# Kernel optimization log

Hardware: AMD Instinct MI355X
Metric: run time of the kernel (lower is better)

The kernel has to match this reference:

```python
import jax, jax.numpy as jnp
import numpy as np

B, T, F, K = 32, 1500, 512, 31
QBITS = 8
EPS = 1e-5


def fake_quant(x, bits=QBITS):
    """Symmetric per-tensor fake quantization (scale from dynamic max-abs),
    with straight-through estimator so gradients pass through unchanged."""
    qmax = 2.0 ** (bits - 1) - 1.0  # 127 for 8 bits
    scale = jnp.maximum(jnp.max(jnp.abs(x)) / qmax, 1e-8)
    q = jnp.clip(jnp.round(x / scale), -qmax - 1.0, qmax) * scale
    return x + jax.lax.stop_gradient(q - x)


def setup_inputs() -> dict:
    key = jax.random.key(0)
    ks = jax.random.split(key, 5)
    x = jax.random.normal(ks[0], (B, T, F), dtype=jnp.float32)
    W1 = jax.random.normal(ks[1], (2 * F, F), dtype=jnp.float32) * (1.0 / np.sqrt(F))
    b1 = jnp.zeros((2 * F,), jnp.float32)
    dw_w = jax.random.normal(ks[2], (F, 1, K), dtype=jnp.float32) * (1.0 / np.sqrt(K))
    dw_b = jnp.zeros((F,), jnp.float32)
    W2 = jax.random.normal(ks[3], (F, F), dtype=jnp.float32) * (1.0 / np.sqrt(F))
    b2 = jnp.zeros((F,), jnp.float32)
    return {
        "x": x,
        "ln_gamma": jnp.ones((F,), jnp.float32),
        "ln_beta": jnp.zeros((F,), jnp.float32),
        "W1": W1, "b1": b1,
        "dw_w": dw_w, "dw_b": dw_b,
        "bn_gamma": jnp.ones((F,), jnp.float32),
        "bn_beta": jnp.zeros((F,), jnp.float32),
        "W2": W2, "b2": b2,
    }


def _forward(x, ln_gamma, ln_beta, W1, b1, dw_w, dw_b, bn_gamma, bn_beta, W2, b2):
    # LayerNorm over last dim F
    mu = jnp.mean(x, axis=-1, keepdims=True)
    var = jnp.mean(jnp.square(x - mu), axis=-1, keepdims=True)
    t = (x - mu) * jax.lax.rsqrt(var + EPS) * ln_gamma + ln_beta

    # pconv1 in-quant -> quantized pointwise conv1 (Linear F -> 2F) -> out-quant
    t = fake_quant(t)
    t = jnp.einsum("btf,gf->btg", t, fake_quant(W1)) + b1
    t = fake_quant(t)

    # GLU over last dim: [B,T,2F] -> [B,T,F]
    a, g = jnp.split(t, 2, axis=-1)
    t = a * jax.nn.sigmoid(g)

    # depthwise conv on [B,F,T]
    t = jnp.transpose(t, (0, 2, 1))  # [B,F,T]
    t = fake_quant(t)
    t = jax.lax.conv_general_dilated(
        t, fake_quant(dw_w),
        window_strides=(1,),
        padding=[((K - 1) // 2, (K - 1) // 2)],
        feature_group_count=F,
        dimension_numbers=("NCH", "OIH", "NCH"),
    ) + dw_b[None, :, None]
    t = fake_quant(t)

    # BatchNorm1d over channel dim (stats over batch and time), training-style batch stats
    bmu = jnp.mean(t, axis=(0, 2), keepdims=True)
    bvar = jnp.mean(jnp.square(t - bmu), axis=(0, 2), keepdims=True)
    t = (t - bmu) * jax.lax.rsqrt(bvar + EPS) * bn_gamma[None, :, None] + bn_beta[None, :, None]

    t = jnp.transpose(t, (0, 2, 1))  # [B,T,F]
    t = jax.nn.silu(t)

    # pconv2 in-quant -> quantized pointwise conv2 (Linear F -> F) -> out-quant
    t = fake_quant(t)
    t = jnp.einsum("btf,gf->btg", t, fake_quant(W2)) + b2
    t = fake_quant(t)
    return t  # dropout is identity (p=0 / eval)


def reference(x, ln_gamma, ln_beta, W1, b1, dw_w, dw_b, bn_gamma, bn_beta, W2, b2):
    return _forward(x, ln_gamma, ln_beta, W1, b1, dw_w, dw_b, bn_gamma, bn_beta, W2, b2)
```

## Files before the change

kernel.cpp:

```cpp
#include <hip/hip_runtime.h>
#include <stdint.h>

typedef __bf16 bf16;
typedef __bf16   bf16x4 __attribute__((ext_vector_type(4)));
typedef __bf16   bf16x8 __attribute__((ext_vector_type(8)));
typedef short    s16x8  __attribute__((ext_vector_type(8)));
typedef float    fx4    __attribute__((ext_vector_type(4)));

#define NB 32
#define NT 1500
#define NF 512
#define NM (NB*NT)
#define KW 31
#define EPSF 1e-5f

__device__ __forceinline__ float dscale(const float* a) {
  return fmaxf(a[0] * (1.0f/127.0f), 1e-8f);
}
__device__ __forceinline__ float fq_int(float x, float inv_s) {
  return fminf(fmaxf(rintf(x*inv_s), -128.0f), 127.0f);
}
__device__ __forceinline__ void block_amax(float v, float* dst) {
  __shared__ float red[8];
  #pragma unroll
  for (int o = 32; o > 0; o >>= 1) v = fmaxf(v, __shfl_xor(v, o));
  if ((threadIdx.x & 63) == 0) red[threadIdx.x >> 6] = v;
  __syncthreads();
  if (threadIdx.x == 0) {
    int nw = blockDim.x >> 6;
    float m = red[0];
    for (int i = 1; i < nw; i++) m = fmaxf(m, red[i]);
    atomicMax((unsigned int*)dst, __float_as_uint(m));
  }
}

__device__ __forceinline__ float amax_loop(const float* p, long n4, int bid, int gsz) {
  float am = 0.f;
  long i = (long)bid * blockDim.x + threadIdx.x;
  long stride = (long)gsz * blockDim.x;
  for (; i < n4; i += stride) {
    fx4 v = ((const fx4*)p)[i];
    #pragma unroll
    for (int j = 0; j < 4; j++) am = fmaxf(am, fabsf(v[j]));
  }
  return am;
}
__global__ void absmax_w(const float* __restrict__ W1, const float* __restrict__ W2,
                         const float* __restrict__ dwp, float* a) {
  int bx = blockIdx.x;
  float am; float* dst;
  if (bx < 256)      { am = amax_loop(W1,  131072, bx,       256); dst = a + 1; }
  else if (bx < 384) { am = amax_loop(W2,  65536,  bx - 256, 128); dst = a + 2; }
  else               { am = amax_loop(dwp, 3968,   bx - 384, 8);   dst = a + 3; }
  block_amax(am, dst);
}

__global__ void quant_pack(const float* __restrict__ src, bf16* __restrict__ dst,
                           int R, const float* amax) {
  float inv_s = 1.0f / dscale(amax);
  int total = R * 64;
  for (int t = blockIdx.x*blockDim.x + threadIdx.x; t < total; t += gridDim.x*blockDim.x) {
    int r = t >> 6, q8 = t & 63;
    const float* s = src + (size_t)r*512 + q8*8;
    fx4 v0 = *(const fx4*)s, v1 = *(const fx4*)(s+4);
    bf16x8 o;
    #pragma unroll
    for (int j = 0; j < 4; j++) { o[j] = (bf16)fq_int(v0[j], inv_s); o[4+j] = (bf16)fq_int(v1[j], inv_s); }
    int r16 = r >> 4, m16 = r & 15, kb = q8 >> 2, quad = q8 & 3;
    size_t chunk = ((size_t)r16*16 + kb)*64 + quad*16 + m16;
    ((bf16x8*)dst)[chunk] = o;
  }
}

__global__ void quant_deq_f32(float* __restrict__ p, long n4, const float* amax) {
  float s = dscale(amax);
  float inv_s = 1.0f / s;
  long i = (long)blockIdx.x * blockDim.x + threadIdx.x;
  long stride = (long)gridDim.x * blockDim.x;
  for (; i < n4; i += stride) {
    fx4 v = ((fx4*)p)[i];
    fx4 o;
    #pragma unroll
    for (int j = 0; j < 4; j++) o[j] = fq_int(v[j], inv_s) * s;
    ((fx4*)p)[i] = o;
  }
}

__global__ void ln_amax_k(const float* __restrict__ x, const float* __restrict__ g,
                          const float* __restrict__ be, float* amax) {
  int lane = threadIdx.x & 63;
  int wavesTotal = (gridDim.x * blockDim.x) >> 6;
  int wave = ((blockIdx.x * blockDim.x) + threadIdx.x) >> 6;
  fx4 g0 = ((const fx4*)g)[2*lane],  g1 = ((const fx4*)g)[2*lane+1];
  fx4 b0 = ((const fx4*)be)[2*lane], b1v = ((const fx4*)be)[2*lane+1];
  float gf[8], bff[8];
  #pragma unroll
  for (int j = 0; j < 4; j++) { gf[j] = g0[j]; gf[4+j] = g1[j]; bff[j] = b0[j]; bff[4+j] = b1v[j]; }
  float am = 0.f;
  for (int row = wave; row < NM; row += wavesTotal) {
    const fx4* xr = (const fx4*)(x + (long)row*NF);
    fx4 x0 = xr[2*lane], x1 = xr[2*lane+1];
    float xf[8]; float s = 0.f;
    #pragma unroll
    for (int j = 0; j < 4; j++) { xf[j] = x0[j]; xf[4+j] = x1[j]; }
    #pragma unroll
    for (int j = 0; j < 8; j++) s += xf[j];
    #pragma unroll
    for (int o = 32; o > 0; o >>= 1) s += __shfl_xor(s, o);
    float mu = s * (1.0f/NF);
    float vs = 0.f;
    #pragma unroll
    for (int j = 0; j < 8; j++) { float d = xf[j]-mu; vs += d*d; }
    #pragma unroll
    for (int o = 32; o > 0; o >>= 1) vs += __shfl_xor(vs, o);
    float inv = rsqrtf(vs*(1.0f/NF) + EPSF);
    #pragma unroll
    for (int j = 0; j < 8; j++) {
      float v = (xf[j]-mu)*inv*gf[j] + bff[j];
      am = fmaxf(am, fabsf(v));
    }
  }
  block_amax(am, amax);
}

__global__ void ln_pack_k(const float* __restrict__ x, const float* __restrict__ g,
                          const float* __restrict__ be, bf16* __restrict__ dst,
                          const float* amax) {
  int lane = threadIdx.x & 63;
  int wavesTotal = (gridDim.x * blockDim.x) >> 6;
  int wave = ((blockIdx.x * blockDim.x) + threadIdx.x) >> 6;
  float inv_s = 1.0f / dscale(amax);
  fx4 g0 = ((const fx4*)g)[2*lane],  g1 = ((const fx4*)g)[2*lane+1];
  fx4 b0 = ((const fx4*)be)[2*lane], b1v = ((const fx4*)be)[2*lane+1];
  float gf[8], bff[8];
  #pragma unroll
  for (int j = 0; j < 4; j++) { gf[j] = g0[j]; gf[4+j] = g1[j]; bff[j] = b0[j]; bff[4+j] = b1v[j]; }
  for (int row = wave; row < NM; row += wavesTotal) {
    const fx4* xr = (const fx4*)(x + (long)row*NF);
    fx4 x0 = xr[2*lane], x1 = xr[2*lane+1];
    float xf[8]; float s = 0.f;
    #pragma unroll
    for (int j = 0; j < 4; j++) { xf[j] = x0[j]; xf[4+j] = x1[j]; }
    #pragma unroll
    for (int j = 0; j < 8; j++) s += xf[j];
    #pragma unroll
    for (int o = 32; o > 0; o >>= 1) s += __shfl_xor(s, o);
    float mu = s * (1.0f/NF);
    float vs = 0.f;
    #pragma unroll
    for (int j = 0; j < 8; j++) { float d = xf[j]-mu; vs += d*d; }
    #pragma unroll
    for (int o = 32; o > 0; o >>= 1) vs += __shfl_xor(vs, o);
    float inv = rsqrtf(vs*(1.0f/NF) + EPSF);
    bf16x8 o8;
    #pragma unroll
    for (int j = 0; j < 8; j++) {
      float v = (xf[j]-mu)*inv*gf[j] + bff[j];
      o8[j] = (bf16)fq_int(v, inv_s);
    }
    int r16 = row >> 4, m16 = row & 15;
    size_t chunk = ((size_t)r16*16 + (lane>>2))*64 + (lane&3)*16 + m16;
    ((bf16x8*)dst)[chunk] = o8;
  }
}

template<int NBN, int MODE>
__global__ __launch_bounds__(256) void gemm_k(
    const bf16* __restrict__ A, const bf16* __restrict__ Bt,
    const float* __restrict__ bias, float* __restrict__ C,
    const float* amaxA, const float* amaxB, float* amaxC) {
  const int N = NBN * 128;
  int id = blockIdx.x;
  int bn = (id >> 3) % NBN;
  int bm = 8 * (id / (8 * NBN)) + (id & 7);
  if (bm >= 375) return;
  int lane = threadIdx.x & 63;
  int w = threadIdx.x >> 6;
  int wm = w >> 1, wn = w & 1;
  int quad = lane >> 4;
  int m16 = lane & 15;

  __shared__ __align__(16) float ebuf[2][32][132];

  fx4 acc[4][4];
  #pragma unroll
  for (int i = 0; i < 4; i++)
    #pragma unroll
    for (int j = 0; j < 4; j++) acc[i][j] = fx4{0.f,0.f,0.f,0.f};

  const bf16* pA[4];
  const bf16* pB[4];
  #pragma unroll
  for (int i = 0; i < 4; i++)
    pA[i] = A + ((size_t)(bm*8 + wm*4 + i)*16)*512 + lane*8;
  #pragma unroll
  for (int j = 0; j < 4; j++)
    pB[j] = Bt + ((size_t)(bn*8 + wn*4 + j)*16)*512 + lane*8;

  s16x8 aC[4], bC[4], aN[4], bN[4];
  #pragma unroll
  for (int i = 0; i < 4; i++) aC[i] = *(const s16x8*)(pA[i]);
  #pragma unroll
  for (int j = 0; j < 4; j++) bC[j] = *(const s16x8*)(pB[j]);

  #pragma unroll
  for (int kb = 0; kb < 16; kb++) {
    if (kb < 15) {
      #pragma unroll
      for (int i = 0; i < 4; i++) aN[i] = *(const s16x8*)(pA[i] + (kb+1)*512);
      #pragma unroll
      for (int j = 0; j < 4; j++) bN[j] = *(const s16x8*)(pB[j] + (kb+1)*512);
    }
    #pragma unroll
    for (int i = 0; i < 4; i++)
      #pragma unroll
      for (int j = 0; j < 4; j++) {
        if (MODE == 0)
          acc[i][j] = __builtin_amdgcn_mfma_f32_16x16x32_bf16(aC[i], bC[j], acc[i][j], 0, 0, 0);
        else
          acc[i][j] = __builtin_amdgcn_mfma_f32_16x16x32_bf16(bC[j], aC[i], acc[i][j], 0, 0, 0);
      }
    __builtin_amdgcn_sched_group_barrier(0x20, 8, 0);
    __builtin_amdgcn_sched_group_barrier(0x8, 16, 0);
    if (kb < 15) {
      #pragma unroll
      for (int i = 0; i < 4; i++) { aC[i] = aN[i]; bC[i] = bN[i]; }
    }
  }

  float ab = dscale(amaxA) * dscale(amaxB);
  float am = 0.f;
  const int h     = (MODE == 0) ? wn : wm;
  const int other = (MODE == 0) ? wm : wn;

  #pragma unroll
  for (int rnd = 0; rnd < 2; rnd++) {
    __syncthreads();
    if (MODE == 0) {
      #pragma unroll
      for (int jj = 0; jj < 2; jj++) {
        int j = rnd*2 + jj;
        int col = bn*128 + wn*64 + j*16 + m16;
        float bv = bias[col];
        #pragma unroll
        for (int i = 0; i < 4; i++) {
          fx4 o;
          #pragma unroll
          for (int rr = 0; rr < 4; rr++) {
            float v = acc[i][j][rr]*ab + bv;
            am = fmaxf(am, fabsf(v)); o[rr] = v;
          }
          *(fx4*)&ebuf[h][jj*16 + m16][wm*64 + i*16 + quad*4] = o;
        }
      }
    } else {
      #pragma unroll
      for (int ii = 0; ii < 2; ii++) {
        int i = rnd*2 + ii;
        #pragma unroll
        for (int j = 0; j < 4; j++) {
          int n0 = bn*128 + wn*64 + j*16 + quad*4;
          fx4 bv = *(const fx4*)(bias + n0);
          fx4 o;
          #pragma unroll
          for (int rr = 0; rr < 4; rr++) {
            float v = acc[i][j][rr]*ab + bv[rr];
            am = fmaxf(am, fabsf(v)); o[rr] = v;
          }
          *(fx4*)&ebuf[h][ii*16 + m16][wn*64 + j*16 + quad*4] = o;
        }
      }
    }
    __syncthreads();
    #pragma unroll
    for (int it = 0; it < 8; it++) {
      int lrow = other*16 + it*2 + (lane >> 5);
      int cf = (lane & 31) * 4;
      fx4 o = *(const fx4*)&ebuf[h][lrow][cf];
      int orow = ((MODE == 0) ? bn*128 : bm*128) + h*64 + rnd*32 + lrow;
      size_t base = (MODE == 0) ? ((size_t)orow*NM + (size_t)bm*128 + cf)
                                : ((size_t)orow*N  + (size_t)bn*128 + cf);
      *(fx4*)(C + base) = o;
    }
  }
  block_amax(am, amaxC);
}

__global__ void glu_k(const float* __restrict__ uT, float* __restrict__ v,
                      const float* amaxU, float* amaxV) {
  float s = dscale(amaxU);
  float inv_s = 1.0f / s;
  float am = 0.f;
  const int tid = threadIdx.x;
  const int npairs = (NB*NF)/2;
  for (int pr = blockIdx.x; pr < npairs; pr += gridDim.x) {
    int row0 = pr*2;
    for (int i = tid; i < 750; i += 256) {
      int r2 = (i >= 375) ? 1 : 0;
      int c = i - 375*r2;
      int row = row0 + r2;
      int b = row >> 9, f = row & (NF-1);
      long bt = (long)b*NT + c*4;
      fx4 a = *(const fx4*)(uT + (long)f*NM + bt);
      fx4 g = *(const fx4*)(uT + (long)(f+NF)*NM + bt);
      fx4 o;
      #pragma unroll
      for (int j = 0; j < 4; j++) {
        float av = fq_int(a[j], inv_s) * s;
        float gv = fq_int(g[j], inv_s) * s;
        float val = av * (1.0f/(1.0f + expf(-gv)));
        am = fmaxf(am, fabsf(val));
        o[j] = val;
      }
      *(fx4*)(v + (long)row*NT + c*4) = o;
    }
  }
  block_amax(am, amaxV);
}

__global__ void dwconv_k(const float* __restrict__ v, const float* __restrict__ w,
                         const float* __restrict__ wb, float* __restrict__ y,
                         const float* amaxV, const float* amaxW, float* amaxY) {
  __shared__ float z[2][1568];
  __shared__ float wl[2][32];
  float sv = dscale(amaxV); float inv_sv = 1.0f/sv;
  float sw = dscale(amaxW); float inv_sw = 1.0f/sw;
  float am = 0.f;
  const int tid = threadIdx.x;
  const int rr = tid >> 7;
  const int cl = tid & 127;
  const int npairs = (NB*NF)/2;
  for (int pr = blockIdx.x; pr < npairs; pr += gridDim.x) {
    int row0 = pr*2;
    __syncthreads();
    if (tid < 64) {
      int r2 = tid >> 5, k = tid & 31;
      if (k < KW) {
        int f = (row0 + r2) & (NF-1);
        wl[r2][k] = fq_int(w[f*KW + k], inv_sw) * sw;
      }
    }
    if (tid < 128) {
      int r2 = tid >> 6, jj = tid & 63;
      if (jj < 16) z[r2][jj] = 0.f;
      else         z[r2][1500 + jj] = 0.f;
    }
    const fx4* vp = (const fx4*)(v + (long)row0 * NT);
    for (int i = tid; i < 750; i += 256) {
      fx4 q = vp[i];
      int r2 = (i >= 375) ? 1 : 0;
      int ii = i - 375*r2;
      fx4 o;
      #pragma unroll
      for (int j = 0; j < 4; j++) o[j] = fq_int(q[j], inv_sv) * sv;
      *(fx4*)&z[r2][16 + 4*ii] = o;
    }
    __syncthreads();
    float wr[KW];
    #pragma unroll
    for (int k = 0; k < KW; k++) wr[k] = wl[rr][k];
    float bias = wb[(row0 + rr) & (NF-1)];
    long base = (long)(row0 + rr) * NT;
    #pragma unroll
    for (int pass = 0; pass < 3; pass++) {
      int c = cl + pass*128;
      if (c < 375) {
        int t0 = c*4;
        fx4 win[9];
        #pragma unroll
        for (int i = 0; i < 9; i++) win[i] = *(const fx4*)&z[rr][t0 + 4*i];
        float acc0 = bias, acc1 = bias, acc2 = bias, acc3 = bias;
        #pragma unroll
        for (int k = 0; k < KW; k++) {
          float wk = wr[k];
          acc0 += win[(k+1)>>2][(k+1)&3] * wk;
          acc1 += win[(k+2)>>2][(k+2)&3] * wk;
          acc2 += win[(k+3)>>2][(k+3)&3] * wk;
          acc3 += win[(k+4)>>2][(k+4)&3] * wk;
        }
        fx4 o = {acc0, acc1, acc2, acc3};
        #pragma unroll
        for (int j = 0; j < 4; j++) am = fmaxf(am, fabsf(o[j]));
        *(fx4*)&y[base + t0] = o;
      }
    }
  }
  block_amax(am, amaxY);
}

__global__ void bnstats_part_k(const float* __restrict__ y, const float* amaxY,
                               int* s1a, int* s2a, unsigned* qmxa, unsigned* qmna) {
  float sy = dscale(amaxY); float inv_sy = 1.0f/sy;
  int f = blockIdx.x & 511;
  int part = blockIdx.x >> 9;
  int s1 = 0, s2 = 0, qmn = 127, qmx = -128;
  for (int b = part*8; b < part*8 + 8; b++) {
    const fx4* base = (const fx4*)(y + ((long)b*NF + f)*NT);
    for (int i = threadIdx.x; i < NT/4; i += blockDim.x) {
      fx4 v = base[i];
      #pragma unroll
      for (int j = 0; j < 4; j++) {
        int q = (int)fq_int(v[j], inv_sy);
        s1 += q; s2 += q*q;
        qmn = min(qmn, q); qmx = max(qmx, q);
      }
    }
  }
  #pragma unroll
  for (int o = 32; o > 0; o >>= 1) {
    s1 += __shfl_xor(s1, o); s2 += __shfl_xor(s2, o);
    qmn = min(qmn, __shfl_xor(qmn, o)); qmx = max(qmx, __shfl_xor(qmx, o));
  }
  __shared__ int rs1[4], rs2[4], rmn[4], rmx[4];
  if ((threadIdx.x & 63) == 0) {
    int wv = threadIdx.x >> 6;
    rs1[wv] = s1; rs2[wv] = s2; rmn[wv] = qmn; rmx[wv] = qmx;
  }
  __syncthreads();
  if (threadIdx.x == 0) {
    int S1 = rs1[0]+rs1[1]+rs1[2]+rs1[3];
    int S2 = rs2[0]+rs2[1]+rs2[2]+rs2[3];
    int mn = min(min(rmn[0],rmn[1]), min(rmn[2],rmn[3]));
    int mx = max(max(rmx[0],rmx[1]), max(rmx[2],rmx[3]));
    atomicAdd(s1a + f, S1);
    atomicAdd(s2a + f, S2);
    atomicMax(qmxa + f, (unsigned)(mx + 128));
    atomicMax(qmna + f, (unsigned)(127 - mn));
  }
}

__global__ void bnfin_k(const int* __restrict__ s1a, const int* __restrict__ s2a,
                        const unsigned* __restrict__ qmxa, const unsigned* __restrict__ qmna,
                        const float* amaxY, const float* __restrict__ bg,
                        const float* __restrict__ bb,
                        float* bn_mean, float* bn_rinv, float* amaxP) {
  int f = blockIdx.x;
  float sy = dscale(amaxY);
  __shared__ float sh_mean, sh_rinv; __shared__ int sh_qmn, sh_qmx;
  if (threadIdx.x == 0) {
    long long S1 = s1a[f];
    long long S2 = s2a[f];
    double s = (double)sy;
    double mean = (double)S1 * s / (double)NM;
    double var  = (double)S2 * s * s / (double)NM - mean*mean;
    float fm = (float)mean;
    float fr = rsqrtf((float)var + EPSF);
    bn_mean[f] = fm; bn_rinv[f] = fr;
    sh_mean = fm; sh_rinv = fr;
    sh_qmx = (int)qmxa[f] - 128;
    sh_qmn = 127 - (int)qmna[f];
  }
  __syncthreads();
  float pm = 0.f;
  int q = sh_qmn + (int)threadIdx.x;
  if (q <= sh_qmx) {
    float zq = (float)q * sy;
    float val = (zq - sh_mean)*sh_rinv*bg[f] + bb[f];
    val = val / (1.0f + expf(-val));
    pm = fabsf(val);
  }
  block_amax(pm, amaxP);
}

__global__ void bnsilu_pack_k(const float* __restrict__ y, const float* __restrict__ bg,
                              const float* __restrict__ bb, const float* amaxY,
                              const float* bn_mean, const float* bn_rinv,
                              bf16* __restrict__ pq, const float* amaxP) {
  __shared__ float lds[32][33];
  float sy = dscale(amaxY); float inv_sy = 1.0f/sy;
  float inv_sp = 1.0f / dscale(amaxP);
  int tx = threadIdx.x & 31, ty = threadIdx.x >> 5;
  const int TTILES = (NT + 31)/32;
  const int ntile = NB * (NF/32) * TTILES;
  for (int tile = blockIdx.x; tile < ntile; tile += gridDim.x) {
    int b = tile / ((NF/32)*TTILES);
    int rem = tile % ((NF/32)*TTILES);
    int fT = rem / TTILES, tT = rem % TTILES;
    int f0 = fT*32, t0 = tT*32;
    __syncthreads();
    #pragma unroll
    for (int sI = 0; sI < 4; sI++) {
      int f = f0 + ty + sI*8;
      int t = t0 + tx;
      if (t < NT) {
        float zq = fq_int(y[((long)b*NF + f)*NT + t], inv_sy) * sy;
        float val = (zq - bn_mean[f])*bn_rinv[f]*bg[f] + bb[f];
        val = val / (1.0f + expf(-val));
        lds[tx][ty + sI*8] = val;
      }
    }
    __syncthreads();
    if (threadIdx.x < 128) {
      int r = threadIdx.x >> 2;
      int c = threadIdx.x & 3;
      int t = t0 + r;
      if (t < NT) {
        bf16x8 o8;
        #pragma unroll
        for (int j = 0; j < 8; j++) o8[j] = (bf16)fq_int(lds[r][c*8 + j], inv_sp);
        long bt = (long)b*NT + t;
        int q8 = (f0 >> 3) + c;
        size_t chunk = ((size_t)(bt>>4)*16 + (q8>>2))*64 + (q8&3)*16 + (bt&15);
        ((bf16x8*)pq)[chunk] = o8;
      }
    }
  }
}

extern "C" void kernel_launch(void* const* d_in, const int* in_sizes, int n_in,
                              void* d_out, int out_size, void* d_ws, size_t ws_size,
                              hipStream_t stream) {
  const float* x  = (const float*)d_in[0];
  const float* lg = (const float*)d_in[1];
  const float* lb = (const float*)d_in[2];
  const float* W1 = (const float*)d_in[3];
  const float* b1 = (const float*)d_in[4];
  const float* dw = (const float*)d_in[5];
  const float* db = (const float*)d_in[6];
  const float* bg = (const float*)d_in[7];
  const float* bb = (const float*)d_in[8];
  const float* W2 = (const float*)d_in[9];
  const float* b2 = (const float*)d_in[10];
  float* out = (float*)d_out;

  char* ws = (char*)d_ws;
  float* amax    = (float*)ws;
  float* bn_mean = (float*)(ws + 1024);
  float* bn_rinv = (float*)(ws + 4096);
  int*      s1a  = (int*)(ws + 8192);
  int*      s2a  = (int*)(ws + 10240);
  unsigned* qmxa = (unsigned*)(ws + 12288);
  unsigned* qmna = (unsigned*)(ws + 14336);
  char* H = ws + 16384;
  float* uT    = (float*)H;
  bf16*  t_q   = (bf16*)(H + 196608000);
  float* y     = (float*)H;
  bf16*  p_q   = (bf16*)(H + 196608000);
  bf16*  W1q   = (bf16*)(H + 245760000);
  bf16*  W2q   = (bf16*)(H + 246808576);
  float* v = (float*)d_out;
  float* r = (float*)d_out;

  hipMemsetAsync(ws, 0, 16384, stream);

  absmax_w<<<392, 256, 0, stream>>>(W1, W2, dw, amax);
  quant_pack<<<256, 256, 0, stream>>>(W1, W1q, 1024, amax+1);
  quant_pack<<<128, 256, 0, stream>>>(W2, W2q, 512,  amax+2);

  ln_amax_k<<<1536, 256, 0, stream>>>(x, lg, lb, amax+0);
  ln_pack_k<<<3072, 256, 0, stream>>>(x, lg, lb, t_q, amax+0);
  gemm_k<8,0><<<3008, 256, 0, stream>>>(t_q, W1q, b1, uT, amax+0, amax+1, amax+4);
  glu_k<<<4096, 256, 0, stream>>>(uT, v, amax+4, amax+5);
  dwconv_k<<<2048, 256, 0, stream>>>(v, dw, db, y, amax+5, amax+3, amax+6);
  bnstats_part_k<<<2048, 256, 0, stream>>>(y, amax+6, s1a, s2a, qmxa, qmna);
  bnfin_k<<<512, 256, 0, stream>>>(s1a, s2a, qmxa, qmna, amax+6, bg, bb, bn_mean, bn_rinv, amax+7);
  bnsilu_pack_k<<<4096, 256, 0, stream>>>(y, bg, bb, amax+6, bn_mean, bn_rinv, p_q, amax+7);
  gemm_k<4,1><<<1504, 256, 0, stream>>>(p_q, W2q, b2, r, amax+7, amax+2, amax+8);
  quant_deq_f32<<<2048, 256, 0, stream>>>(out, 24576000/4, amax+8);
}
```

Baseline: 600.9 us.

## Stage GEMM operands through LDS with triple-buffered direct global-to-LDS loads

The GEMM main loop no longer loads A/B fragments straight from global memory into registers. It now issues asynchronous global_load_lds copies into a 3-deep shared-memory ring and synchronises with explicit vmcnt waits and barriers. The goal is to keep more loads in flight, lower register pressure and hide memory latency, at the cost of two block barriers per k-step. Separately, the dwconv launch grid grows from 2048 to 8192 blocks, which only works if that kernel already loops in a grid-stride style.

```diff
diff --git a/kernel.cpp b/kernel.cpp
--- a/kernel.cpp
+++ b/kernel.cpp
@@ -180,7 +180,7 @@
   int quad = lane >> 4;
   int m16 = lane & 15;
 
-  __shared__ __align__(16) float ebuf[2][32][132];
+  __shared__ __align__(16) char smem[49152];
 
   fx4 acc[4][4];
   #pragma unroll
@@ -188,45 +188,58 @@
     #pragma unroll
     for (int j = 0; j < 4; j++) acc[i][j] = fx4{0.f,0.f,0.f,0.f};
 
-  const bf16* pA[4];
-  const bf16* pB[4];
-  #pragma unroll
-  for (int i = 0; i < 4; i++)
-    pA[i] = A + ((size_t)(bm*8 + wm*4 + i)*16)*512 + lane*8;
-  #pragma unroll
-  for (int j = 0; j < 4; j++)
-    pB[j] = Bt + ((size_t)(bn*8 + wn*4 + j)*16)*512 + lane*8;
-
-  s16x8 aC[4], bC[4], aN[4], bN[4];
-  #pragma unroll
-  for (int i = 0; i < 4; i++) aC[i] = *(const s16x8*)(pA[i]);
-  #pragma unroll
-  for (int j = 0; j < 4; j++) bC[j] = *(const s16x8*)(pB[j]);
+  const bf16* gA = A  + (size_t)(bm*8)*16*512;
+  const bf16* gB = Bt + (size_t)(bn*8)*16*512;
+
+  auto issue = [&](int kb) {
+    int b = kb % 3;
+    #pragma unroll
+    for (int q = 0; q < 4; q++) {
+      int p = w*4 + q;
+      const bf16* src = (p < 8)
+          ? (gA + (size_t)p*8192     + (size_t)kb*512 + lane*8)
+          : (gB + (size_t)(p-8)*8192 + (size_t)kb*512 + lane*8);
+      __builtin_amdgcn_global_load_lds(
+          (const __attribute__((address_space(1))) void*)src,
+          (__attribute__((address_space(3))) void*)(smem + b*16384 + p*1024 + lane*16),
+          16, 0, 0);
+    }
+  };
+
+  issue(0); issue(1); issue(2);
 
   #pragma unroll
   for (int kb = 0; kb < 16; kb++) {
-    if (kb < 15) {
-      #pragma unroll
-      for (int i = 0; i < 4; i++) aN[i] = *(const s16x8*)(pA[i] + (kb+1)*512);
-      #pragma unroll
-      for (int j = 0; j < 4; j++) bN[j] = *(const s16x8*)(pB[j] + (kb+1)*512);
-    }
+    if (kb <= 13)      asm volatile("s_waitcnt vmcnt(8)" ::: "memory");
+    else if (kb == 14) asm volatile("s_waitcnt vmcnt(4)" ::: "memory");
+    else               asm volatile("s_waitcnt vmcnt(0)" ::: "memory");
+    __builtin_amdgcn_sched_barrier(0);
+    __builtin_amdgcn_s_barrier();
+    __builtin_amdgcn_sched_barrier(0);
+    char* buf = smem + (kb % 3)*16384;
+    s16x8 aF[4], bF[4];
+    #pragma unroll
+    for (int i = 0; i < 4; i++) aF[i] = *(const s16x8*)(buf + (wm*4 + i)*1024 + lane*16);
+    #pragma unroll
+    for (int j = 0; j < 4; j++) bF[j] = *(const s16x8*)(buf + (8 + wn*4 + j)*1024 + lane*16);
     #pragma unroll
     for (int i = 0; i < 4; i++)
       #pragma unroll
       for (int j = 0; j < 4; j++) {
         if (MODE == 0)
-          acc[i][j] = __builtin_amdgcn_mfma_f32_16x16x32_bf16(aC[i], bC[j], acc[i][j], 0, 0, 0);
+          acc[i][j] = __builtin_amdgcn_mfma_f32_16x16x32_bf16(aF[i], bF[j], acc[i][j], 0, 0, 0);
         else
-          acc[i][j] = __builtin_amdgcn_mfma_f32_16x16x32_bf16(bC[j], aC[i], acc[i][j], 0, 0, 0);
-      }
-    __builtin_amdgcn_sched_group_barrier(0x20, 8, 0);
-    __builtin_amdgcn_sched_group_barrier(0x8, 16, 0);
-    if (kb < 15) {
-      #pragma unroll
-      for (int i = 0; i < 4; i++) { aC[i] = aN[i]; bC[i] = bN[i]; }
-    }
-  }
+          acc[i][j] = __builtin_amdgcn_mfma_f32_16x16x32_bf16(bF[j], aF[i], acc[i][j], 0, 0, 0);
+      }
+    asm volatile("s_waitcnt lgkmcnt(0)" ::: "memory");
+    __builtin_amdgcn_sched_barrier(0);
+    __builtin_amdgcn_s_barrier();
+    __builtin_amdgcn_sched_barrier(0);
+    if (kb + 3 < 16) issue(kb + 3);
+  }
+  __syncthreads();
+
+  float (*ebuf)[32][132] = (float (*)[32][132])smem;
 
   float ab = dscale(amaxA) * dscale(amaxB);
   float am = 0.f;
@@ -551,7 +564,7 @@
   ln_pack_k<<<3072, 256, 0, stream>>>(x, lg, lb, t_q, amax+0);
   gemm_k<8,0><<<3008, 256, 0, stream>>>(t_q, W1q, b1, uT, amax+0, amax+1, amax+4);
   glu_k<<<4096, 256, 0, stream>>>(uT, v, amax+4, amax+5);
-  dwconv_k<<<2048, 256, 0, stream>>>(v, dw, db, y, amax+5, amax+3, amax+6);
+  dwconv_k<<<8192, 256, 0, stream>>>(v, dw, db, y, amax+5, amax+3, amax+6);
   bnstats_part_k<<<2048, 256, 0, stream>>>(y, amax+6, s1a, s2a, qmxa, qmna);
   bnfin_k<<<512, 256, 0, stream>>>(s1a, s2a, qmxa, qmna, amax+6, bg, bb, bn_mean, bn_rinv, amax+7);
   bnsilu_pack_k<<<4096, 256, 0, stream>>>(y, bg, bb, amax+6, bn_mean, bn_rinv, p_q, amax+7);
```

New measurement: 723.6 us. +20.4%, slower.

## Switch quantized GEMMs from bf16 MFMA to int8 MFMA with packed layouts

Applied to the files above, without the earlier changes.

Quantized activations and weights are now packed as int8 instead of bf16 integer values. Both GEMMs use the i32 16x16x64 int8 MFMA and convert the integer accumulators to float in the epilogue. This halves operand bytes and the number of K iterations, and int8 MFMA has higher peak throughput than bf16. The explicit register double-buffering and scheduling barriers are removed, which may expose load latency, and the depthwise conv grid is enlarged.

```diff
diff --git a/kernel.cpp b/kernel.cpp
--- a/kernel.cpp
+++ b/kernel.cpp
@@ -2,10 +2,9 @@
 #include <stdint.h>
 
 typedef __bf16 bf16;
-typedef __bf16   bf16x4 __attribute__((ext_vector_type(4)));
-typedef __bf16   bf16x8 __attribute__((ext_vector_type(8)));
-typedef short    s16x8  __attribute__((ext_vector_type(8)));
 typedef float    fx4    __attribute__((ext_vector_type(4)));
+typedef int      ix2    __attribute__((ext_vector_type(2)));
+typedef int      ix4    __attribute__((ext_vector_type(4)));
 
 #define NB 32
 #define NT 1500
@@ -55,20 +54,25 @@
   block_amax(am, dst);
 }
 
-__global__ void quant_pack(const float* __restrict__ src, bf16* __restrict__ dst,
-                           int R, const float* amax) {
+__global__ void quant_pack_i8(const float* __restrict__ src, char* __restrict__ dst,
+                              int R, const float* amax) {
   float inv_s = 1.0f / dscale(amax);
-  int total = R * 64;
+  int total = R * 32;
   for (int t = blockIdx.x*blockDim.x + threadIdx.x; t < total; t += gridDim.x*blockDim.x) {
-    int r = t >> 6, q8 = t & 63;
-    const float* s = src + (size_t)r*512 + q8*8;
-    fx4 v0 = *(const fx4*)s, v1 = *(const fx4*)(s+4);
-    bf16x8 o;
-    #pragma unroll
-    for (int j = 0; j < 4; j++) { o[j] = (bf16)fq_int(v0[j], inv_s); o[4+j] = (bf16)fq_int(v1[j], inv_s); }
-    int r16 = r >> 4, m16 = r & 15, kb = q8 >> 2, quad = q8 & 3;
-    size_t chunk = ((size_t)r16*16 + kb)*64 + quad*16 + m16;
-    ((bf16x8*)dst)[chunk] = o;
+    int r = t >> 5, q16 = t & 31;
+    const float* s = src + (size_t)r*512 + q16*16;
+    ix4 o;
+    #pragma unroll
+    for (int g = 0; g < 4; g++) {
+      fx4 v = *(const fx4*)(s + g*4);
+      int wrd = 0;
+      #pragma unroll
+      for (int j = 0; j < 4; j++) wrd |= ((int)fq_int(v[j], inv_s) & 0xff) << (8*j);
+      o[g] = wrd;
+    }
+    int r16 = r >> 4, m16 = r & 15, kb = q16 >> 2, quad = q16 & 3;
+    size_t chunk = ((size_t)r16*8 + kb)*64 + quad*16 + m16;
+    ((ix4*)dst)[chunk] = o;
   }
 }
 
@@ -124,7 +128,7 @@
 }
 
 __global__ void ln_pack_k(const float* __restrict__ x, const float* __restrict__ g,
-                          const float* __restrict__ be, bf16* __restrict__ dst,
+                          const float* __restrict__ be, char* __restrict__ dst,
                           const float* amax) {
   int lane = threadIdx.x & 63;
   int wavesTotal = (gridDim.x * blockDim.x) >> 6;
@@ -152,21 +156,25 @@
     #pragma unroll
     for (int o = 32; o > 0; o >>= 1) vs += __shfl_xor(vs, o);
     float inv = rsqrtf(vs*(1.0f/NF) + EPSF);
-    bf16x8 o8;
-    #pragma unroll
-    for (int j = 0; j < 8; j++) {
+    int lo = 0, hi = 0;
+    #pragma unroll
+    for (int j = 0; j < 4; j++) {
       float v = (xf[j]-mu)*inv*gf[j] + bff[j];
-      o8[j] = (bf16)fq_int(v, inv_s);
-    }
-    int r16 = row >> 4, m16 = row & 15;
-    size_t chunk = ((size_t)r16*16 + (lane>>2))*64 + (lane&3)*16 + m16;
-    ((bf16x8*)dst)[chunk] = o8;
+      lo |= ((int)fq_int(v, inv_s) & 0xff) << (8*j);
+    }
+    #pragma unroll
+    for (int j = 0; j < 4; j++) {
+      float v = (xf[4+j]-mu)*inv*gf[4+j] + bff[4+j];
+      hi |= ((int)fq_int(v, inv_s) & 0xff) << (8*j);
+    }
+    size_t chunk = ((size_t)(row>>4)*8 + (lane>>3))*64 + ((lane>>1)&3)*16 + (row&15);
+    *(ix2*)(dst + chunk*16 + (lane&1)*8) = ix2{lo, hi};
   }
 }
 
 template<int NBN, int MODE>
 __global__ __launch_bounds__(256) void gemm_k(
-    const bf16* __restrict__ A, const bf16* __restrict__ Bt,
+    const char* __restrict__ A, const char* __restrict__ Bt,
     const float* __restrict__ bias, float* __restrict__ C,
     const float* amaxA, const float* amaxB, float* amaxC) {
   const int N = NBN * 128;
@@ -182,50 +190,37 @@
 
   __shared__ __align__(16) float ebuf[2][32][132];
 
-  fx4 acc[4][4];
+  ix4 acc[4][4];
   #pragma unroll
   for (int i = 0; i < 4; i++)
     #pragma unroll
-    for (int j = 0; j < 4; j++) acc[i][j] = fx4{0.f,0.f,0.f,0.f};
-
-  const bf16* pA[4];
-  const bf16* pB[4];
+    for (int j = 0; j < 4; j++) acc[i][j] = ix4{0,0,0,0};
+
+  const char* pA[4];
+  const char* pB[4];
   #pragma unroll
   for (int i = 0; i < 4; i++)
-    pA[i] = A + ((size_t)(bm*8 + wm*4 + i)*16)*512 + lane*8;
+    pA[i] = A + (size_t)(bm*8 + wm*4 + i)*8192 + lane*16;
   #pragma unroll
   for (int j = 0; j < 4; j++)
-    pB[j] = Bt + ((size_t)(bn*8 + wn*4 + j)*16)*512 + lane*8;
-
-  s16x8 aC[4], bC[4], aN[4], bN[4];
-  #pragma unroll
-  for (int i = 0; i < 4; i++) aC[i] = *(const s16x8*)(pA[i]);
-  #pragma unroll
-  for (int j = 0; j < 4; j++) bC[j] = *(const s16x8*)(pB[j]);
-
-  #pragma unroll
-  for (int kb = 0; kb < 16; kb++) {
-    if (kb < 15) {
-      #pragma unroll
-      for (int i = 0; i < 4; i++) aN[i] = *(const s16x8*)(pA[i] + (kb+1)*512);
-      #pragma unroll
-      for (int j = 0; j < 4; j++) bN[j] = *(const s16x8*)(pB[j] + (kb+1)*512);
-    }
+    pB[j] = Bt + (size_t)(bn*8 + wn*4 + j)*8192 + lane*16;
+
+  #pragma unroll
+  for (int kb = 0; kb < 8; kb++) {
+    ix4 aF[4], bF[4];
+    #pragma unroll
+    for (int i = 0; i < 4; i++) aF[i] = *(const ix4*)(pA[i] + kb*1024);
+    #pragma unroll
+    for (int j = 0; j < 4; j++) bF[j] = *(const ix4*)(pB[j] + kb*1024);
     #pragma unroll
     for (int i = 0; i < 4; i++)
       #pragma unroll
       for (int j = 0; j < 4; j++) {
         if (MODE == 0)
-          acc[i][j] = __builtin_amdgcn_mfma_f32_16x16x32_bf16(aC[i], bC[j], acc[i][j], 0, 0, 0);
+          acc[i][j] = __builtin_amdgcn_mfma_i32_16x16x64_i8(aF[i], bF[j], acc[i][j], 0, 0, 0);
         else
-          acc[i][j] = __builtin_amdgcn_mfma_f32_16x16x32_bf16(bC[j], aC[i], acc[i][j], 0, 0, 0);
-      }
-    __builtin_amdgcn_sched_group_barrier(0x20, 8, 0);
-    __builtin_amdgcn_sched_group_barrier(0x8, 16, 0);
-    if (kb < 15) {
-      #pragma unroll
-      for (int i = 0; i < 4; i++) { aC[i] = aN[i]; bC[i] = bN[i]; }
-    }
+          acc[i][j] = __builtin_amdgcn_mfma_i32_16x16x64_i8(bF[j], aF[i], acc[i][j], 0, 0, 0);
+      }
   }
 
   float ab = dscale(amaxA) * dscale(amaxB);
@@ -247,7 +242,7 @@
           fx4 o;
           #pragma unroll
           for (int rr = 0; rr < 4; rr++) {
-            float v = acc[i][j][rr]*ab + bv;
+            float v = (float)acc[i][j][rr]*ab + bv;
             am = fmaxf(am, fabsf(v)); o[rr] = v;
           }
           *(fx4*)&ebuf[h][jj*16 + m16][wm*64 + i*16 + quad*4] = o;
@@ -264,7 +259,7 @@
           fx4 o;
           #pragma unroll
           for (int rr = 0; rr < 4; rr++) {
-            float v = acc[i][j][rr]*ab + bv[rr];
+            float v = (float)acc[i][j][rr]*ab + bv[rr];
             am = fmaxf(am, fabsf(v)); o[rr] = v;
           }
           *(fx4*)&ebuf[h][ii*16 + m16][wn*64 + j*16 + quad*4] = o;
@@ -465,7 +460,7 @@
 __global__ void bnsilu_pack_k(const float* __restrict__ y, const float* __restrict__ bg,
                               const float* __restrict__ bb, const float* amaxY,
                               const float* bn_mean, const float* bn_rinv,
-                              bf16* __restrict__ pq, const float* amaxP) {
+                              char* __restrict__ pq, const float* amaxP) {
   __shared__ float lds[32][33];
   float sy = dscale(amaxY); float inv_sy = 1.0f/sy;
   float inv_sp = 1.0f / dscale(amaxP);
@@ -495,13 +490,17 @@
       int c = threadIdx.x & 3;
       int t = t0 + r;
       if (t < NT) {
-        bf16x8 o8;
-        #pragma unroll
-        for (int j = 0; j < 8; j++) o8[j] = (bf16)fq_int(lds[r][c*8 + j], inv_sp);
+        int lo = 0, hi = 0;
+        #pragma unroll
+        for (int j = 0; j < 4; j++)
+          lo |= ((int)fq_int(lds[r][c*8 + j],     inv_sp) & 0xff) << (8*j);
+        #pragma unroll
+        for (int j = 0; j < 4; j++)
+          hi |= ((int)fq_int(lds[r][c*8 + 4 + j], inv_sp) & 0xff) << (8*j);
         long bt = (long)b*NT + t;
         int q8 = (f0 >> 3) + c;
-        size_t chunk = ((size_t)(bt>>4)*16 + (q8>>2))*64 + (q8&3)*16 + (bt&15);
-        ((bf16x8*)pq)[chunk] = o8;
+        size_t chunk = ((size_t)(bt>>4)*8 + (q8>>3))*64 + ((q8>>1)&3)*16 + (bt&15);
+        *(ix2*)(pq + chunk*16 + (q8&1)*8) = ix2{lo, hi};
       }
     }
   }
@@ -533,25 +532,25 @@
   unsigned* qmna = (unsigned*)(ws + 14336);
   char* H = ws + 16384;
   float* uT    = (float*)H;
-  bf16*  t_q   = (bf16*)(H + 196608000);
+  char*  t_q   = H + 196608000;
   float* y     = (float*)H;
-  bf16*  p_q   = (bf16*)(H + 196608000);
-  bf16*  W1q   = (bf16*)(H + 245760000);
-  bf16*  W2q   = (bf16*)(H + 246808576);
+  char*  p_q   = H + 221184000;
+  char*  W1q   = H + 245760000;
+  char*  W2q   = H + 246284288;
   float* v = (float*)d_out;
   float* r = (float*)d_out;
 
   hipMemsetAsync(ws, 0, 16384, stream);
 
   absmax_w<<<392, 256, 0, stream>>>(W1, W2, dw, amax);
-  quant_pack<<<256, 256, 0, stream>>>(W1, W1q, 1024, amax+1);
-  quant_pack<<<128, 256, 0, stream>>>(W2, W2q, 512,  amax+2);
+  quant_pack_i8<<<128, 256, 0, stream>>>(W1, W1q, 1024, amax+1);
+  quant_pack_i8<<<64,  256, 0, stream>>>(W2, W2q, 512,  amax+2);
 
   ln_amax_k<<<1536, 256, 0, stream>>>(x, lg, lb, amax+0);
   ln_pack_k<<<3072, 256, 0, stream>>>(x, lg, lb, t_q, amax+0);
   gemm_k<8,0><<<3008, 256, 0, stream>>>(t_q, W1q, b1, uT, amax+0, amax+1, amax+4);
   glu_k<<<4096, 256, 0, stream>>>(uT, v, amax+4, amax+5);
-  dwconv_k<<<2048, 256, 0, stream>>>(v, dw, db, y, amax+5, amax+3, amax+6);
+  dwconv_k<<<8192, 256, 0, stream>>>(v, dw, db, y, amax+5, amax+3, amax+6);
   bnstats_part_k<<<2048, 256, 0, stream>>>(y, amax+6, s1a, s2a, qmxa, qmna);
   bnfin_k<<<512, 256, 0, stream>>>(s1a, s2a, qmxa, qmna, amax+6, bg, bb, bn_mean, bn_rinv, amax+7);
   bnsilu_pack_k<<<4096, 256, 0, stream>>>(y, bg, bb, amax+6, bn_mean, bn_rinv, p_q, amax+7);
```

Result: no change. 591.4 us (-1.6%).
